# Optimization experiments

Measured on AMD Instinct MI355X. Metric: run time of the kernel, lower is better.

Reference implementation:

```python
import jax, jax.numpy as jnp
import numpy as np

DEGREE = 3
NUM_KNOTS = 64  # max(64, DEGREE + 5)
N_POINTS = 500_000


def _bspline_basis(x, knots, k):
    """Faithful port of BSplineBasis.forward.

    Each basis element i is scipy BSpline.basis_element(knots[i:i+k+2]) with
    extrapolate=True: padded knots T = [t0-1]*k + seg + [tend+1]*k, one-hot
    coefficient at index k. Evaluation = find_interval (clamped to [k, 2k],
    i.e. the element's support pieces, extrapolating outside) + de Boor
    (_deBoor_D) recursion with the xb==xa zero guard.
    x: [N,1]; knots: [num_knots]; returns [N, num_knots-k-1].
    """
    num_knots = knots.shape[0]
    nb = num_knots - k - 1                      # number of basis elements
    xs = jnp.squeeze(x)                          # [N]
    xn = (xs - xs.min()) / (xs.max() - xs.min() + 1e-8)

    # per-element padded knot vectors: [nb, 3k+2]
    seg = knots[jnp.arange(nb)[:, None] + jnp.arange(k + 2)[None, :]]  # [nb, k+2]
    T = jnp.concatenate([
        jnp.repeat(seg[:, :1] - 1.0, k, axis=1),
        seg,
        jnp.repeat(seg[:, -1:] + 1.0, k, axis=1),
    ], axis=1)

    # interval index per (element, point), clamped to base-interval pieces [k, 2k]
    ell = jnp.clip(
        jax.vmap(lambda t: jnp.searchsorted(t, xn, side='right'))(T) - 1,
        k, 2 * k)                                # [nb, N] int32

    def tg(off):  # T[b, ell + off] -> [nb, N]
        return jnp.take_along_axis(T, ell + off, axis=1)

    xb_ = xn[None, :]                            # [1, N]
    res = [jnp.ones(ell.shape, xn.dtype)] + \
          [jnp.zeros(ell.shape, xn.dtype) for _ in range(k)]

    # scipy _deBoor_D: builds the k+1 non-vanishing B-splines at interval ell
    for j in range(1, k + 1):
        hh = list(res[:j])
        res[0] = jnp.zeros_like(res[0])
        for n in range(1, j + 1):
            tb = tg(n)
            ta = tg(n - j)
            den = tb - ta
            w = jnp.where(den == 0, 0.0,
                          hh[n - 1] / jnp.where(den == 0, 1.0, den))
            res[n - 1] = res[n - 1] + w * (tb - xb_)
            res[n] = w * (xb_ - ta)

    vals = jnp.stack(res, axis=0)                # [k+1, nb, N]
    # one-hot coeff at padded index k -> pick res[2k - ell]
    out = jnp.take_along_axis(vals, (2 * k - ell)[None], axis=0)[0]  # [nb, N]
    return jnp.nan_to_num(out).T                 # [N, nb]


def setup_inputs() -> dict:
    key = jax.random.key(0)
    inner = np.linspace(0.0, 1.0, NUM_KNOTS - 2 * DEGREE)
    knots = np.concatenate([np.zeros(DEGREE), inner, np.ones(DEGREE)]).astype(np.float32)
    x = jax.random.normal(key, (N_POINTS, 1), dtype=jnp.float32)
    return {"x": x, "knots": jnp.asarray(knots), "degree": DEGREE}


def reference(x, knots, degree):
    return _bspline_basis(x, knots, degree)
```

## Files before the change

### kernel.cpp

```cpp
#include <hip/hip_runtime.h>
#include <math.h>

#define NK   64
#define NBAS 60
#define NBLK1 256

__global__ __launch_bounds__(256) void minmax_partial_k(const float* __restrict__ x, int n,
                                                        float2* __restrict__ part) {
    __shared__ float2 red[4];
    int t = threadIdx.x;
    float mn = INFINITY, mx = -INFINITY;
    for (unsigned i = blockIdx.x * 256u + t; i < (unsigned)n; i += 256u * NBLK1) {
        float v = x[i];
        mn = fminf(mn, v);
        mx = fmaxf(mx, v);
    }
    #pragma unroll
    for (int off = 32; off; off >>= 1) {
        mn = fminf(mn, __shfl_xor(mn, off));
        mx = fmaxf(mx, __shfl_xor(mx, off));
    }
    if ((t & 63) == 0) red[t >> 6] = make_float2(mn, mx);
    __syncthreads();
    if (t == 0) {
        mn = fminf(fminf(red[0].x, red[1].x), fminf(red[2].x, red[3].x));
        mx = fmaxf(fmaxf(red[0].y, red[1].y), fmaxf(red[2].y, red[3].y));
        part[blockIdx.x] = make_float2(mn, mx);
    }
}

__global__ __launch_bounds__(256, 4) void bspline_main_k(const float* __restrict__ x,
                                                         const float* __restrict__ knots,
                                                         const float2* __restrict__ part,
                                                         float* __restrict__ out, int np) {
    __shared__ float4 scoef[4 * NBAS];
    __shared__ float2 spt[256];
    __shared__ float2 swred[4];
    int t = threadIdx.x;
    int blockStart = blockIdx.x * 256;

    float2 pr = part[t];
    float mn = pr.x, mx = pr.y;
    #pragma unroll
    for (int off = 32; off; off >>= 1) {
        mn = fminf(mn, __shfl_xor(mn, off));
        mx = fmaxf(mx, __shfl_xor(mx, off));
    }
    if ((t & 63) == 0) swred[t >> 6] = make_float2(mn, mx);

    if (t < 4 * NBAS) {
        int i = t >> 2;
        int m = t & 3;
        float k0 = knots[i], k1 = knots[i + 1], k2 = knots[i + 2],
              k3 = knots[i + 3], k4 = knots[i + 4];
        float tq[6];
        #pragma unroll
        for (int d = 0; d < 6; ++d) {
            int q = m + 1 + d;
            int ci = q - 3; ci = ci < 0 ? 0 : (ci > 4 ? 4 : ci);
            float kv = ci == 0 ? k0 : ci == 1 ? k1 : ci == 2 ? k2 : ci == 3 ? k3 : k4;
            kv += (q < 3) ? -1.0f : ((q > 7) ? 1.0f : 0.0f);
            tq[d] = kv;
        }
        float tm2 = tq[0], tm1 = tq[1], tt0 = tq[2], tt1 = tq[3], tt2 = tq[4], tt3 = tq[5];

        float den = tt1 - tt0;
        float s = (den == 0.0f) ? 0.0f : __builtin_amdgcn_rcpf(den);
        float r0_0 = s * tt1, r0_1 = -s;
        float r1_0 = -s * tt0, r1_1 = s;
        den = tt1 - tm1; s = (den == 0.0f) ? 0.0f : __builtin_amdgcn_rcpf(den);
        float w0 = s * r0_0, w1 = s * r0_1;
        float a0_0 = tt1 * w0, a0_1 = tt1 * w1 - w0, a0_2 = -w1;
        float b1_0 = -tm1 * w0, b1_1 = w0 - tm1 * w1, b1_2 = w1;
        den = tt2 - tt0; s = (den == 0.0f) ? 0.0f : __builtin_amdgcn_rcpf(den);
        w0 = s * r1_0; w1 = s * r1_1;
        float a1_0 = b1_0 + tt2 * w0, a1_1 = b1_1 + tt2 * w1 - w0, a1_2 = b1_2 - w1;
        float a2_0 = -tt0 * w0, a2_1 = w0 - tt0 * w1, a2_2 = w1;
        den = tt1 - tm2; s = (den == 0.0f) ? 0.0f : __builtin_amdgcn_rcpf(den);
        w0 = s * a0_0; w1 = s * a0_1; float w2 = s * a0_2;
        float R0_0 = tt1 * w0, R0_1 = tt1 * w1 - w0, R0_2 = tt1 * w2 - w1, R0_3 = -w2;
        float R1_0 = -tm2 * w0, R1_1 = w0 - tm2 * w1, R1_2 = w1 - tm2 * w2, R1_3 = w2;
        den = tt2 - tm1; s = (den == 0.0f) ? 0.0f : __builtin_amdgcn_rcpf(den);
        w0 = s * a1_0; w1 = s * a1_1; w2 = s * a1_2;
        R1_0 += tt2 * w0; R1_1 += tt2 * w1 - w0; R1_2 += tt2 * w2 - w1; R1_3 -= w2;
        float R2_0 = -tm1 * w0, R2_1 = w0 - tm1 * w1, R2_2 = w1 - tm1 * w2, R2_3 = w2;
        den = tt3 - tt0; s = (den == 0.0f) ? 0.0f : __builtin_amdgcn_rcpf(den);
        w0 = s * a2_0; w1 = s * a2_1; w2 = s * a2_2;
        R2_0 += tt3 * w0; R2_1 += tt3 * w1 - w0; R2_2 += tt3 * w2 - w1; R2_3 -= w2;
        float R3_0 = -tt0 * w0, R3_1 = w0 - tt0 * w1, R3_2 = w1 - tt0 * w2, R3_3 = w2;

        float o0, o1, o2, o3;
        if (m == 0)      { o0 = R3_0; o1 = R3_1; o2 = R3_2; o3 = R3_3; }
        else if (m == 1) { o0 = R2_0; o1 = R2_1; o2 = R2_2; o3 = R2_3; }
        else if (m == 2) { o0 = R1_0; o1 = R1_1; o2 = R1_2; o3 = R1_3; }
        else             { o0 = R0_0; o1 = R0_1; o2 = R0_2; o3 = R0_3; }
        scoef[m * NBAS + i] = make_float4(o0, o1, o2, o3);
    }
    __syncthreads();

    float2 ra = swred[0], rb = swred[1], rc = swred[2], rd = swred[3];
    mn = fminf(fminf(ra.x, rb.x), fminf(rc.x, rd.x));
    mx = fmaxf(fmaxf(ra.y, rb.y), fmaxf(rc.y, rd.y));
    float inv = __builtin_amdgcn_rcpf(mx - mn + 1e-8f);
    int p = blockStart + t;
    int pc = p < np ? p : (np - 1);
    float xn = (x[pc] - mn) * inv;
    int S = 0;
    #pragma unroll
    for (int j = 0; j < NK; ++j) S += (knots[j] <= xn) ? 1 : 0;
    spt[t] = make_float2(xn, __int_as_float(S));
    __syncthreads();

    int pl = t / NBAS;
    int ii = t - pl * NBAS;
    int npl = np - blockStart;
    float* po = out + (long long)blockStart * NBAS + t;
    #pragma unroll 4
    for (int it = 0; it < NBAS; ++it) {
        if (pl < npl) {
            float2 v = spt[pl];
            int S2 = __float_as_int(v.y);
            int m = S2 - 1 - ii; m = m < 0 ? 0 : (m > 3 ? 3 : m);
            float4 cf = scoef[m * NBAS + ii];
            float xv = v.x;
            float r = fmaf(fmaf(fmaf(cf.w, xv, cf.z), xv, cf.y), xv, cf.x);
            __builtin_nontemporal_store(r, po);
        }
        po += 256;
        ii += 16; pl += 4;
        if (ii >= NBAS) { ii -= NBAS; pl += 1; }
    }
}

extern "C" void kernel_launch(void* const* d_in, const int* in_sizes, int n_in,
                              void* d_out, int out_size, void* d_ws, size_t ws_size,
                              hipStream_t stream) {
    const float* x     = (const float*)d_in[0];
    const float* knots = (const float*)d_in[1];
    float* out = (float*)d_out;
    float2* part = (float2*)d_ws;
    int np = in_sizes[0];

    hipLaunchKernelGGL(minmax_partial_k, dim3(NBLK1), dim3(256), 0, stream, x, np, part);
    int blocks = (np + 255) / 256;
    hipLaunchKernelGGL(bspline_main_k, dim3(blocks), dim3(256), 0, stream,
                       x, knots, part, out, np);
}
```

Baseline: 144.3 us.

## Vectorize output stores, hoist coefficient build to prep kernel, double points per block

Moves the per-element polynomial coefficient computation out of every main-kernel block into block 0 of the min/max prep kernel, which writes the coefficients to workspace. The main kernel now copies them into shared memory. Each block now handles 512 points instead of 256, and each thread writes 4 consecutive output floats as one 128-bit nontemporal store instead of scalar stores. The goal is to cut redundant per-block arithmetic and make the write-bound output stream more efficient, at the cost of per-element division and index wrapping in the store loop.

```diff
diff --git a/kernel.cpp b/kernel.cpp
--- a/kernel.cpp
+++ b/kernel.cpp
@@ -1,12 +1,18 @@
 #include <hip/hip_runtime.h>
 #include <math.h>
 
-#define NK   64
-#define NBAS 60
+#define NK    64
+#define NBAS  60
 #define NBLK1 256
+#define PPB   512
 
-__global__ __launch_bounds__(256) void minmax_partial_k(const float* __restrict__ x, int n,
-                                                        float2* __restrict__ part) {
+typedef float floatx4 __attribute__((ext_vector_type(4)));
+
+
+__global__ __launch_bounds__(256) void prep_k(const float* __restrict__ x, int n,
+                                              const float* __restrict__ knots,
+                                              float2* __restrict__ part,
+                                              float4* __restrict__ coef) {
     __shared__ float2 red[4];
     int t = threadIdx.x;
     float mn = INFINITY, mx = -INFINITY;
@@ -27,28 +33,8 @@
         mx = fmaxf(fmaxf(red[0].y, red[1].y), fmaxf(red[2].y, red[3].y));
         part[blockIdx.x] = make_float2(mn, mx);
     }
-}
 
-__global__ __launch_bounds__(256, 4) void bspline_main_k(const float* __restrict__ x,
-                                                         const float* __restrict__ knots,
-                                                         const float2* __restrict__ part,
-                                                         float* __restrict__ out, int np) {
-    __shared__ float4 scoef[4 * NBAS];
-    __shared__ float2 spt[256];
-    __shared__ float2 swred[4];
-    int t = threadIdx.x;
-    int blockStart = blockIdx.x * 256;
-
-    float2 pr = part[t];
-    float mn = pr.x, mx = pr.y;
-    #pragma unroll
-    for (int off = 32; off; off >>= 1) {
-        mn = fminf(mn, __shfl_xor(mn, off));
-        mx = fmaxf(mx, __shfl_xor(mx, off));
-    }
-    if ((t & 63) == 0) swred[t >> 6] = make_float2(mn, mx);
-
-    if (t < 4 * NBAS) {
+    if (blockIdx.x == 0 && t < 4 * NBAS) {
         int i = t >> 2;
         int m = t & 3;
         float k0 = knots[i], k1 = knots[i + 1], k2 = knots[i + 2],
@@ -94,41 +80,77 @@
         else if (m == 1) { o0 = R2_0; o1 = R2_1; o2 = R2_2; o3 = R2_3; }
         else if (m == 2) { o0 = R1_0; o1 = R1_1; o2 = R1_2; o3 = R1_3; }
         else             { o0 = R0_0; o1 = R0_1; o2 = R0_2; o3 = R0_3; }
-        scoef[m * NBAS + i] = make_float4(o0, o1, o2, o3);
+        coef[m * NBAS + i] = make_float4(o0, o1, o2, o3);
     }
+}
+
+__global__ __launch_bounds__(256, 6) void bspline_main_k(const float* __restrict__ x,
+                                                         const float* __restrict__ knots,
+                                                         const float2* __restrict__ part,
+                                                         const float4* __restrict__ coef,
+                                                         float* __restrict__ out, int np) {
+    __shared__ float4 scoef[4 * NBAS];
+    __shared__ float2 spt[PPB];
+    __shared__ float2 swred[4];
+    int t = threadIdx.x;
+    int blockStart = blockIdx.x * PPB;
+
+    if (t < 4 * NBAS) scoef[t] = coef[t];
+    float2 pr = part[t];
+    float mn = pr.x, mx = pr.y;
+    #pragma unroll
+    for (int off = 32; off; off >>= 1) {
+        mn = fminf(mn, __shfl_xor(mn, off));
+        mx = fmaxf(mx, __shfl_xor(mx, off));
+    }
+    if ((t & 63) == 0) swred[t >> 6] = make_float2(mn, mx);
     __syncthreads();
 
     float2 ra = swred[0], rb = swred[1], rc = swred[2], rd = swred[3];
     mn = fminf(fminf(ra.x, rb.x), fminf(rc.x, rd.x));
     mx = fmaxf(fmaxf(ra.y, rb.y), fmaxf(rc.y, rd.y));
     float inv = __builtin_amdgcn_rcpf(mx - mn + 1e-8f);
-    int p = blockStart + t;
-    int pc = p < np ? p : (np - 1);
-    float xn = (x[pc] - mn) * inv;
-    int S = 0;
+
+    int npl = np - blockStart;
+    if (npl > PPB) npl = PPB;
+
     #pragma unroll
-    for (int j = 0; j < NK; ++j) S += (knots[j] <= xn) ? 1 : 0;
-    spt[t] = make_float2(xn, __int_as_float(S));
+    for (int s = 0; s < 2; ++s) {
+        int p = blockStart + s * 256 + t;
+        int pc = p < np ? p : (np - 1);
+        float xn = (x[pc] - mn) * inv;
+        int S = 0;
+        #pragma unroll
+        for (int j = 0; j < NK; ++j) S += (knots[j] <= xn) ? 1 : 0;
+        spt[s * 256 + t] = make_float2(xn, __int_as_float(S));
+    }
     __syncthreads();
 
-    int pl = t / NBAS;
-    int ii = t - pl * NBAS;
-    int npl = np - blockStart;
-    float* po = out + (long long)blockStart * NBAS + t;
-    #pragma unroll 4
-    for (int it = 0; it < NBAS; ++it) {
-        if (pl < npl) {
-            float2 v = spt[pl];
-            int S2 = __float_as_int(v.y);
-            int m = S2 - 1 - ii; m = m < 0 ? 0 : (m > 3 ? 3 : m);
-            float4 cf = scoef[m * NBAS + ii];
-            float xv = v.x;
-            float r = fmaf(fmaf(fmaf(cf.w, xv, cf.z), xv, cf.y), xv, cf.x);
-            __builtin_nontemporal_store(r, po);
+    int nout = npl * NBAS;
+    floatx4* po = (floatx4*)(out + (long long)blockStart * NBAS);
+    #pragma unroll 2
+    for (int it = 0; it < (PPB * NBAS) / 1024; ++it) {
+        int f = it * 1024 + (t << 2);
+        if (f < nout) {
+            unsigned pl0 = (unsigned)f / 60u;
+            int ii0 = f - (int)pl0 * 60;
+            float2 v0 = spt[pl0];
+            float2 v1 = spt[pl0 + (pl0 < PPB - 1 ? 1u : 0u)];
+            float r[4];
+            #pragma unroll
+            for (int c = 0; c < 4; ++c) {
+                int ii = ii0 + c;
+                int wz = (ii >= NBAS) ? 1 : 0;
+                ii -= wz * NBAS;
+                float xv = wz ? v1.x : v0.x;
+                int S2 = __float_as_int(wz ? v1.y : v0.y);
+                int m = S2 - 1 - ii; m = m < 0 ? 0 : (m > 3 ? 3 : m);
+                float4 cf = scoef[m * NBAS + ii];
+                r[c] = fmaf(fmaf(fmaf(cf.w, xv, cf.z), xv, cf.y), xv, cf.x);
+            }
+            floatx4 rv = { r[0], r[1], r[2], r[3] };
+            __builtin_nontemporal_store(rv, po + it * 256 + t);
         }
-        po += 256;
-        ii += 16; pl += 4;
-        if (ii >= NBAS) { ii -= NBAS; pl += 1; }
     }
 }
 
@@ -139,10 +161,11 @@
     const float* knots = (const float*)d_in[1];
     float* out = (float*)d_out;
     float2* part = (float2*)d_ws;
+    float4* coef = (float4*)((char*)d_ws + 2048);
     int np = in_sizes[0];
 
-    hipLaunchKernelGGL(minmax_partial_k, dim3(NBLK1), dim3(256), 0, stream, x, np, part);
-    int blocks = (np + 255) / 256;
+    hipLaunchKernelGGL(prep_k, dim3(NBLK1), dim3(256), 0, stream, x, np, knots, part, coef);
+    int blocks = (np + PPB - 1) / PPB;
     hipLaunchKernelGGL(bspline_main_k, dim3(blocks), dim3(256), 0, stream,
-                       x, knots, part, out, np);
+                       x, knots, part, coef, out, np);
 }
```

Result: no change. 143.2 us (-0.8%).
